# Performance work log

Hardware: AMD Instinct MI355X
Metric: run time of the kernel (lower is better)

## Reference

```python
import jax, jax.numpy as jnp
import numpy as np

B, S, H = 2, 2048, 2048
NH, KVH, HD = 32, 8, 64
G = NH // KVH
BASE = 10000.0
SCALE = 1.0 / np.sqrt(HD).astype(np.float32)


def _rope_cache(seq_len, dim, base):
    inv_freq = 1.0 / (base ** (jnp.arange(0, dim, 2, dtype=jnp.float32) / dim))
    t = jnp.arange(seq_len, dtype=jnp.float32)
    freqs = jnp.outer(t, inv_freq)            # [S, HD/2]
    emb = jnp.concatenate([freqs, freqs], -1)  # [S, HD]
    return jnp.cos(emb), jnp.sin(emb)


def _rotate_half(x):
    x1, x2 = jnp.split(x, 2, axis=-1)
    return jnp.concatenate([-x2, x1], axis=-1)


def setup_inputs() -> dict:
    key = jax.random.key(0)
    ks = jax.random.split(key, 5)
    hidden_states = jax.random.normal(ks[0], (B, S, H), jnp.float32)
    # additive causal mask, broadcast over heads
    causal = jnp.tril(jnp.ones((S, S), dtype=bool))
    attention_mask = jnp.where(causal, 0.0, -1e9).astype(jnp.float32)[None, None]
    attention_mask = jnp.broadcast_to(attention_mask, (B, 1, S, S))
    position_ids = jnp.broadcast_to(jnp.arange(S, dtype=jnp.int32), (B, S))
    w = 0.02
    Wq = jax.random.normal(ks[1], (H, NH * HD), jnp.float32) * w
    Wk = jax.random.normal(ks[2], (H, KVH * HD), jnp.float32) * w
    Wv = jax.random.normal(ks[3], (H, KVH * HD), jnp.float32) * w
    Wo = jax.random.normal(ks[4], (NH * HD, H), jnp.float32) * w
    return {"hidden_states": hidden_states, "attention_mask": attention_mask,
            "position_ids": position_ids, "Wq": Wq, "Wk": Wk, "Wv": Wv, "Wo": Wo}


def reference(hidden_states, attention_mask, position_ids, Wq, Wk, Wv, Wo):
    b, s, _ = hidden_states.shape
    q = (hidden_states @ Wq).reshape(b, s, NH, HD).transpose(0, 2, 1, 3)   # [B,NH,S,HD]
    k = (hidden_states @ Wk).reshape(b, s, KVH, HD).transpose(0, 2, 1, 3)  # [B,KVH,S,HD]
    v = (hidden_states @ Wv).reshape(b, s, KVH, HD).transpose(0, 2, 1, 3)
    cos_c, sin_c = _rope_cache(s, HD, BASE)
    cos = cos_c[position_ids][:, None]  # [B,1,S,HD]
    sin = sin_c[position_ids][:, None]
    q = q * cos + _rotate_half(q) * sin
    k = k * cos + _rotate_half(k) * sin
    # GQA: grouped einsum == repeat_kv + matmul (same math, no KV duplication)
    qg = q.reshape(b, KVH, G, s, HD)
    scores = jnp.einsum('bkgsd,bktd->bkgst', qg, k) * SCALE  # [B,KVH,G,S,S]
    scores = scores + attention_mask[:, :, None]             # mask [B,1,1,S,S]
    probs = jax.nn.softmax(scores.astype(jnp.float32), axis=-1).astype(q.dtype)
    ctx = jnp.einsum('bkgst,bktd->bkgsd', probs, v)
    ctx = ctx.reshape(b, NH, s, HD).transpose(0, 2, 1, 3).reshape(b, s, NH * HD)
    return ctx @ Wo
```

## Files before the change

kernel.cpp:

```cpp
#include <hip/hip_runtime.h>
#include <hip/hip_bf16.h>

#define DB   2
#define DS   2048
#define DH   2048
#define DNH  32
#define DKVH 8
#define DHD  64
#define DM   4096
#define DNQKV 3072

typedef __attribute__((ext_vector_type(8))) short bf16x8;
typedef __attribute__((ext_vector_type(4))) float f32x4;
typedef __attribute__((ext_vector_type(8))) unsigned short us8;
typedef __attribute__((ext_vector_type(4))) unsigned short us4;
typedef __attribute__((ext_vector_type(2))) unsigned int u32x2;

__device__ __forceinline__ float b2f(unsigned short u) {
  unsigned int x = ((unsigned int)u) << 16;
  return __builtin_bit_cast(float, x);
}
__device__ __forceinline__ unsigned short f2b(float f) {
  unsigned int u = __builtin_bit_cast(unsigned int, f);
  return (unsigned short)((u + 0x8000u) >> 16);
}
__device__ __forceinline__ unsigned int cvt_pk_bf16(float lo, float hi) {
  unsigned int r;
  asm("v_cvt_pk_bf16_f32 %0, %1, %2" : "=v"(r) : "v"(lo), "v"(hi));
  return r;
}
__device__ __forceinline__ void async_copy16(void* lds, const void* g) {
  __builtin_amdgcn_global_load_lds((const __attribute__((address_space(1))) void*)g,
                                   (__attribute__((address_space(3))) void*)lds,
                                   16, 0, 0);
}

#define BARRIER() do { asm volatile("" ::: "memory"); __builtin_amdgcn_s_barrier(); asm volatile("" ::: "memory"); } while (0)
#define LGKM0()   asm volatile("s_waitcnt lgkmcnt(0)" ::: "memory")
#define WAITVM(n) asm volatile("s_waitcnt vmcnt(" #n ")" ::: "memory")
#define MFMA16(d, a, bb) (d) = __builtin_amdgcn_mfma_f32_16x16x32_bf16((a), (bb), (d), 0, 0, 0)

__device__ __forceinline__ int detect_inline(const unsigned short* __restrict__ w) {
  int t = threadIdx.x & 63;
  int trips = 0;
#pragma unroll
  for (int i = 0; i < 4; i++) {
    unsigned short u = w[t * 4 + i];
    int e = (u >> 7) & 0xFF;
    if (e >= 161 || (e <= 93 && e != 0)) trips++;
  }
#pragma unroll
  for (int off = 32; off > 0; off >>= 1) trips += __shfl_down(trips, off);
  return __shfl(trips, 0) >= 8;
}

__global__ __launch_bounds__(256)
void prep(const void* __restrict__ hs, const void* __restrict__ wq,
          const void* __restrict__ wk, const void* __restrict__ wv,
          const void* __restrict__ wo,
          unsigned short* __restrict__ xb, unsigned short* __restrict__ wtqkv,
          unsigned short* __restrict__ wto) {
  __shared__ float tile[32][33];
  int mode = detect_inline((const unsigned short*)wq);
  int bid = blockIdx.x;
  if (bid < 4096) {
    int i = (bid * 256 + threadIdx.x) * 8;
    if (mode) {
      const float* f = (const float*)hs;
      us8 o;
#pragma unroll
      for (int j = 0; j < 8; j++) o[j] = f2b(f[i + j]);
      *(us8*)&xb[i] = o;
    } else {
      *(us8*)&xb[i] = *(const us8*)((const unsigned short*)hs + i);
    }
    return;
  }
  const void* win; unsigned short* out; int C, bx, by;
  if (bid < 8192)       { int l = bid - 4096;  win = wq; out = wtqkv;                         C = 2048; bx = l & 63; by = l >> 6; }
  else if (bid < 9216)  { int l = bid - 8192;  win = wk; out = wtqkv + (size_t)2048 * 2048;   C = 512;  bx = l & 15; by = l >> 4; }
  else if (bid < 10240) { int l = bid - 9216;  win = wv; out = wtqkv + (size_t)2560 * 2048;   C = 512;  bx = l & 15; by = l >> 4; }
  else                  { int l = bid - 10240; win = wo; out = wto;                           C = 2048; bx = l & 63; by = l >> 6; }
  int c0 = bx * 32, r0 = by * 32;
  int tx = threadIdx.x & 31, ty = threadIdx.x >> 5;
  if (mode) {
    const float* f = (const float*)win;
    for (int i = ty; i < 32; i += 8) tile[i][tx] = f[(size_t)(r0 + i) * C + c0 + tx];
  } else {
    const unsigned short* bsrc = (const unsigned short*)win;
    for (int i = ty; i < 32; i += 8) tile[i][tx] = b2f(bsrc[(size_t)(r0 + i) * C + c0 + tx]);
  }
  __syncthreads();
  for (int i = ty; i < 32; i += 8) out[(size_t)(c0 + i) * 2048 + r0 + tx] = f2b(tile[tx][i]);
}

#define QSC 0.18033688011112042f

__global__ __launch_bounds__(512, 2)
void gemm_qkv(const unsigned short* __restrict__ A, const unsigned short* __restrict__ Bt,
              const int* __restrict__ pos_ids,
              unsigned short* __restrict__ qws, unsigned short* __restrict__ kws,
              unsigned short* __restrict__ vt) {
  __shared__ __align__(16) unsigned short sm[65536];
  int tid = threadIdx.x, lane = tid & 63, wave = tid >> 6;
  int wm = wave >> 2, wn = wave & 3;
  int quad = lane >> 4, l15 = lane & 15;

  int bid = blockIdx.x;
  int wg = (bid & 7) * 24 + (bid >> 3);
  int ty = wg / 12, tx = wg - ty * 12;
  size_t tm0 = (size_t)ty * 256, tn0 = (size_t)tx * 256;

  const unsigned short* Ab = A + tm0 * 2048;
  const unsigned short* Bb = Bt + tn0 * 2048;

  auto UA = [&](int bu, int kh) { return sm + (bu * 2 + kh) * 8192; };
  auto UB = [&](int bu, int kh) { return sm + 32768 + (bu * 2 + kh) * 8192; };

  int c0 = tid, c1 = tid + 512;
  int r0s = c0 >> 2, r1s = c1 >> 2;
  int cc0 = (c0 & 3) ^ ((r0s >> 1) & 3);
  int cc1 = (c1 & 3) ^ ((r1s >> 1) & 3);
  size_t ga0 = (size_t)r0s * 2048 + cc0 * 8;
  size_t ga1 = (size_t)r1s * 2048 + cc1 * 8;

  auto stA = [&](int t, int kh, int bu) {
    const unsigned short* s = Ab + (size_t)t * 64 + kh * 32;
    async_copy16(UA(bu, kh) + c0 * 8, s + ga0);
    async_copy16(UA(bu, kh) + c1 * 8, s + ga1);
  };
  auto stB = [&](int t, int kh, int bu) {
    const unsigned short* s = Bb + (size_t)t * 64 + kh * 32;
    async_copy16(UB(bu, kh) + c0 * 8, s + ga0);
    async_copy16(UB(bu, kh) + c1 * 8, s + ga1);
  };

  int rdoff = l15 * 32 + ((quad << 3) ^ (((l15 >> 1) & 3) << 3));

  f32x4 zero4 = {0.f, 0.f, 0.f, 0.f};
  f32x4 acc[8][4];
#pragma unroll
  for (int mi = 0; mi < 8; mi++)
#pragma unroll
    for (int ni = 0; ni < 4; ni++) acc[mi][ni] = zero4;

  stA(0, 0, 0); stB(0, 0, 0); stA(0, 1, 0); stB(0, 1, 0); stA(1, 0, 1); stB(1, 0, 1);
  WAITVM(8); BARRIER();

#pragma unroll 2
  for (int t = 0; t < 32; ++t) {
    int bu = t & 1, bn = bu ^ 1;
    int t1 = (t + 1 < 32) ? t + 1 : 31;
    int t2 = (t + 2 < 32) ? t + 2 : 31;
    bf16x8 af[8];
    const unsigned short* pA0 = UA(bu, 0) + wm * 4096 + rdoff;
    const unsigned short* pB0 = UB(bu, 0) + wn * 2048 + rdoff;
    const unsigned short* pA1 = UA(bu, 1) + wm * 4096 + rdoff;
    const unsigned short* pB1 = UB(bu, 1) + wn * 2048 + rdoff;

#pragma unroll
    for (int mi = 0; mi < 8; mi++) af[mi] = *(const bf16x8*)(pA0 + mi * 512);
    bf16x8 b0 = *(const bf16x8*)pB0;
    bf16x8 b1 = *(const bf16x8*)(pB0 + 512);
    stA(t1, 1, bn);
    BARRIER(); LGKM0();
    __builtin_amdgcn_s_setprio(1);
#pragma unroll
    for (int mi = 0; mi < 8; mi++) { MFMA16(acc[mi][0], af[mi], b0); MFMA16(acc[mi][1], af[mi], b1); }
    __builtin_amdgcn_s_setprio(0);
    BARRIER();

    bf16x8 b2 = *(const bf16x8*)(pB0 + 1024);
    bf16x8 b3 = *(const bf16x8*)(pB0 + 1536);
    stB(t1, 1, bn);
    BARRIER(); LGKM0();
    __builtin_amdgcn_s_setprio(1);
#pragma unroll
    for (int mi = 0; mi < 8; mi++) { MFMA16(acc[mi][2], af[mi], b2); MFMA16(acc[mi][3], af[mi], b3); }
    __builtin_amdgcn_s_setprio(0);
    WAITVM(8);
    BARRIER();

#pragma unroll
    for (int mi = 0; mi < 8; mi++) af[mi] = *(const bf16x8*)(pA1 + mi * 512);
    b0 = *(const bf16x8*)pB1;
    b1 = *(const bf16x8*)(pB1 + 512);
    stA(t2, 0, bu);
    BARRIER(); LGKM0();
    __builtin_amdgcn_s_setprio(1);
#pragma unroll
    for (int mi = 0; mi < 8; mi++) { MFMA16(acc[mi][0], af[mi], b0); MFMA16(acc[mi][1], af[mi], b1); }
    __builtin_amdgcn_s_setprio(0);
    BARRIER();

    b2 = *(const bf16x8*)(pB1 + 1024);
    b3 = *(const bf16x8*)(pB1 + 1536);
    stB(t2, 0, bu);
    BARRIER(); LGKM0();
    __builtin_amdgcn_s_setprio(1);
#pragma unroll
    for (int mi = 0; mi < 8; mi++) { MFMA16(acc[mi][2], af[mi], b2); MFMA16(acc[mi][3], af[mi], b3); }
    __builtin_amdgcn_s_setprio(0);
    WAITVM(8);
    BARRIER();
  }
  WAITVM(0);

  int hs = (int)(tn0 >> 6) + wn;
  if (hs < 40) {
    float sc = (hs < 32) ? QSC : 1.0f;
    unsigned short* dst0 = (hs < 32) ? qws : kws;
    int hh = (hs < 32) ? hs : (hs - 32);
    float invf0 = __expf(-(float)l15 * (9.210340371976184f / 32.0f));
    float invf1 = invf0 * 0.01f;
#pragma unroll
    for (int mi = 0; mi < 8; mi++)
#pragma unroll
      for (int r = 0; r < 4; r++) {
        size_t gr = tm0 + wm * 128 + mi * 16 + quad * 4 + r;
        int bb = (int)(gr >> 11), s = (int)(gr & 2047);
        float tpos = (float)pos_ids[gr];
        unsigned short* row = dst0 + ((size_t)(bb * ((hs < 32) ? DNH : DKVH) + hh) * DS + s) * DHD;
#pragma unroll
        for (int ni = 0; ni < 2; ni++) {
          float x1 = acc[mi][ni][r], x2 = acc[mi][ni + 2][r];
          float ang = tpos * (ni ? invf1 : invf0);
          float sn, cs;
          __sincosf(ang, &sn, &cs);
          int d = ni * 16 + l15;
          row[d]      = f2b((x1 * cs - x2 * sn) * sc);
          row[d + 32] = f2b((x2 * cs + x1 * sn) * sc);
        }
      }
  } else {
    int vh = hs - 40;
    int bb = (int)(tm0 >> 11);
    int s0 = (int)(tm0 & 2047) + wm * 128 + quad * 4;
#pragma unroll
    for (int mi = 0; mi < 8; mi++)
#pragma unroll
      for (int ni = 0; ni < 4; ni++) {
        int d = ni * 16 + l15;
        us4 o4;
#pragma unroll
        for (int r = 0; r < 4; r++) o4[r] = f2b(acc[mi][ni][r]);
        *(us4*)&vt[((size_t)(bb * DKVH + vh) * DHD + d) * DS + s0 + mi * 16] = o4;
      }
  }
}

__global__ __launch_bounds__(512, 2)
void gemm_out(const unsigned short* __restrict__ A, const unsigned short* __restrict__ Bt,
              unsigned short* __restrict__ Cb, float* __restrict__ Cf,
              const unsigned short* __restrict__ wqdet) {
  __shared__ __align__(16) unsigned short sm[49152];
  int tid = threadIdx.x, lane = tid & 63, wave = tid >> 6;
  int wm = wave >> 2, wn = wave & 3;
  int quad = lane >> 4, l15 = lane & 15;

  int bid = blockIdx.x;
  int wg = (bid & 7) * 32 + (bid >> 3);
  int ty = wg >> 3, tx = wg & 7;
  size_t tm0 = (size_t)ty * 128, tn0 = (size_t)tx * 256;

  const unsigned short* Ab = A + tm0 * 2048;
  const unsigned short* Bb = Bt + tn0 * 2048;

  auto UA = [&](int bu, int kh) { return sm + (bu * 2 + kh) * 4096; };
  auto UB = [&](int bu, int kh) { return sm + 16384 + (bu * 2 + kh) * 8192; };

  int c0 = tid, c1 = tid + 512;
  int r0s = c0 >> 2, r1s = c1 >> 2;
  int cc0 = (c0 & 3) ^ ((r0s >> 1) & 3);
  int cc1 = (c1 & 3) ^ ((r1s >> 1) & 3);
  size_t ga0 = (size_t)r0s * 2048 + cc0 * 8;
  size_t ga1 = (size_t)r1s * 2048 + cc1 * 8;

  auto stA = [&](int t, int kh, int bu) {
    const unsigned short* s = Ab + (size_t)t * 64 + kh * 32;
    async_copy16(UA(bu, kh) + c0 * 8, s + ga0);
  };
  auto stB = [&](int t, int kh, int bu) {
    const unsigned short* s = Bb + (size_t)t * 64 + kh * 32;
    async_copy16(UB(bu, kh) + c0 * 8, s + ga0);
    async_copy16(UB(bu, kh) + c1 * 8, s + ga1);
  };

  int rdoff = l15 * 32 + ((quad << 3) ^ (((l15 >> 1) & 3) << 3));

  f32x4 zero4 = {0.f, 0.f, 0.f, 0.f};
  f32x4 acc[4][4];
#pragma unroll
  for (int mi = 0; mi < 4; mi++)
#pragma unroll
    for (int ni = 0; ni < 4; ni++) acc[mi][ni] = zero4;

  stA(0, 0, 0); stB(0, 0, 0); stA(0, 1, 0); stB(0, 1, 0); stA(1, 0, 1); stB(1, 0, 1);
  WAITVM(6); BARRIER();

#pragma unroll 2
  for (int t = 0; t < 32; ++t) {
    int bu = t & 1, bn = bu ^ 1;
    int t1 = (t + 1 < 32) ? t + 1 : 31;
    int t2 = (t + 2 < 32) ? t + 2 : 31;
    bf16x8 af[4];
    const unsigned short* pA0 = UA(bu, 0) + wm * 2048 + rdoff;
    const unsigned short* pB0 = UB(bu, 0) + wn * 2048 + rdoff;
    const unsigned short* pA1 = UA(bu, 1) + wm * 2048 + rdoff;
    const unsigned short* pB1 = UB(bu, 1) + wn * 2048 + rdoff;

#pragma unroll
    for (int mi = 0; mi < 4; mi++) af[mi] = *(const bf16x8*)(pA0 + mi * 512);
    bf16x8 b0 = *(const bf16x8*)pB0;
    bf16x8 b1 = *(const bf16x8*)(pB0 + 512);
    stA(t1, 1, bn);
    BARRIER(); LGKM0();
    __builtin_amdgcn_s_setprio(1);
#pragma unroll
    for (int mi = 0; mi < 4; mi++) { MFMA16(acc[mi][0], af[mi], b0); MFMA16(acc[mi][1], af[mi], b1); }
    __builtin_amdgcn_s_setprio(0);
    BARRIER();

    bf16x8 b2 = *(const bf16x8*)(pB0 + 1024);
    bf16x8 b3 = *(const bf16x8*)(pB0 + 1536);
    stB(t1, 1, bn);
    BARRIER(); LGKM0();
    __builtin_amdgcn_s_setprio(1);
#pragma unroll
    for (int mi = 0; mi < 4; mi++) { MFMA16(acc[mi][2], af[mi], b2); MFMA16(acc[mi][3], af[mi], b3); }
    __builtin_amdgcn_s_setprio(0);
    WAITVM(6);
    BARRIER();

#pragma unroll
    for (int mi = 0; mi < 4; mi++) af[mi] = *(const bf16x8*)(pA1 + mi * 512);
    b0 = *(const bf16x8*)pB1;
    b1 = *(const bf16x8*)(pB1 + 512);
    stA(t2, 0, bu);
    BARRIER(); LGKM0();
    __builtin_amdgcn_s_setprio(1);
#pragma unroll
    for (int mi = 0; mi < 4; mi++) { MFMA16(acc[mi][0], af[mi], b0); MFMA16(acc[mi][1], af[mi], b1); }
    __builtin_amdgcn_s_setprio(0);
    BARRIER();

    b2 = *(const bf16x8*)(pB1 + 1024);
    b3 = *(const bf16x8*)(pB1 + 1536);
    stB(t2, 0, bu);
    BARRIER(); LGKM0();
    __builtin_amdgcn_s_setprio(1);
#pragma unroll
    for (int mi = 0; mi < 4; mi++) { MFMA16(acc[mi][2], af[mi], b2); MFMA16(acc[mi][3], af[mi], b3); }
    __builtin_amdgcn_s_setprio(0);
    WAITVM(6);
    BARRIER();
  }
  WAITVM(0);

  int mode = detect_inline(wqdet);
#pragma unroll
  for (int mi = 0; mi < 4; mi++)
#pragma unroll
    for (int ni = 0; ni < 4; ni++)
#pragma unroll
      for (int r = 0; r < 4; r++) {
        size_t gr = tm0 + wm * 64 + mi * 16 + quad * 4 + r;
        size_t gc = tn0 + wn * 64 + ni * 16 + l15;
        float v = acc[mi][ni][r];
        if (mode) Cf[gr * 2048 + gc] = v;
        else      Cb[gr * 2048 + gc] = f2b(v);
      }
}

__global__ __launch_bounds__(256, 4)
void flash_attn(const unsigned short* __restrict__ q, const unsigned short* __restrict__ k,
                const unsigned short* __restrict__ vt, unsigned short* __restrict__ ctx) {
  __shared__ __align__(16) unsigned short lK[2][2][64 * 32];
  __shared__ __align__(16) unsigned short lV[2][2][64 * 32];
  __shared__ __align__(16) unsigned short lP[4][16 * 64];
  int tid = threadIdx.x, lane = tid & 63, wave = tid >> 6;
  int quad = lane >> 4, l15 = lane & 15;
  int bh = blockIdx.y, b = bh >> 5, h = bh & 31, kvh = h >> 2;
  const unsigned short* qb = q + (size_t)(b * DNH + h) * DS * DHD;
  const unsigned short* kb = k + (size_t)(b * DKVH + kvh) * DS * DHD;
  const unsigned short* vb = vt + (size_t)(b * DKVH + kvh) * DHD * DS;
  unsigned short* lPw = lP[wave];
  int r4 = tid >> 2;
  int cc8 = ((tid & 3) ^ ((r4 >> 1) & 3)) * 8;
  int swz = ((l15 >> 1) & 3) << 3;
  int pswz = (l15 & 7) << 3;
  int ql = wave * 16 + l15;

  int qt = blockIdx.x;
  int ntA = qt + 1, ntB = 32 - qt;
  int q0A = qt * 64, q0B = (31 - qt) * 64;

  const unsigned short* qpA = qb + (size_t)(q0A + ql) * DHD + quad * 8;
  const unsigned short* qpB = qb + (size_t)(q0B + ql) * DHD + quad * 8;
  bf16x8 qfA0 = *(const bf16x8*)qpA;
  bf16x8 qfA1 = *(const bf16x8*)(qpA + 32);
  bf16x8 qfB0 = *(const bf16x8*)qpB;
  bf16x8 qfB1 = *(const bf16x8*)(qpB + 32);

  f32x4 zero4 = {0.f, 0.f, 0.f, 0.f};
  f32x4 oA[4], oB[4];
#pragma unroll
  for (int dj = 0; dj < 4; dj++) { oA[dj] = zero4; oB[dj] = zero4; }
  float mA = -1e30f, lA = 0.f, mB = -1e30f, lB = 0.f;

  auto stage = [&](int t, int buf) {
    const unsigned short* sk = kb + (size_t)(t * 64 + r4) * DHD + cc8;
    async_copy16(&lK[buf][0][tid * 8], sk);
    async_copy16(&lK[buf][1][tid * 8], sk + 32);
    const unsigned short* sv = vb + (size_t)r4 * DS + t * 64 + cc8;
    async_copy16(&lV[buf][0][tid * 8], sv);
    async_copy16(&lV[buf][1][tid * 8], sv + 32);
  };

  auto smax_pv = [&](f32x4 (&sacc)[4], float& mrow, float& lrow, f32x4 (&oacc)[4],
                     int cur, int maskdiag) {
    if (maskdiag) {
#pragma unroll
      for (int nj = 0; nj < 4; nj++)
#pragma unroll
        for (int r = 0; r < 4; r++)
          if (nj * 16 + quad * 4 + r > ql) sacc[nj][r] = -1e30f;
    }
    float a0 = fmaxf(fmaxf(sacc[0][0], sacc[0][1]), sacc[0][2]);
    float a1 = fmaxf(fmaxf(sacc[0][3], sacc[1][0]), sacc[1][1]);
    float a2 = fmaxf(fmaxf(sacc[1][2], sacc[1][3]), sacc[2][0]);
    float a3 = fmaxf(fmaxf(sacc[2][1], sacc[2][2]), sacc[2][3]);
    float a4 = fmaxf(fmaxf(sacc[3][0], sacc[3][1]), sacc[3][2]);
    float tm = fmaxf(fmaxf(fmaxf(a0, a1), fmaxf(a2, a3)), fmaxf(a4, sacc[3][3]));
    tm = fmaxf(tm, __shfl_xor(tm, 16));
    tm = fmaxf(tm, __shfl_xor(tm, 32));
    if (!__all(tm <= mrow + 8.f)) {
      float mn = fmaxf(mrow, tm);
      float alpha = __builtin_amdgcn_exp2f(mrow - mn);
      mrow = mn;
      lrow *= alpha;
#pragma unroll
      for (int dj = 0; dj < 4; dj++)
#pragma unroll
        for (int r = 0; r < 4; r++) oacc[dj][r] *= alpha;
    }
    float rs = 0.f;
#pragma unroll
    for (int nj = 0; nj < 4; nj++)
#pragma unroll
      for (int r = 0; r < 4; r++) {
        float e = __builtin_amdgcn_exp2f(sacc[nj][r] - mrow);
        sacc[nj][r] = e;
        rs += e;
      }
    rs += __shfl_xor(rs, 16);
    rs += __shfl_xor(rs, 32);
    lrow += rs;
#pragma unroll
    for (int nj = 0; nj < 4; nj++) {
      u32x2 w2;
      w2[0] = cvt_pk_bf16(sacc[nj][0], sacc[nj][1]);
      w2[1] = cvt_pk_bf16(sacc[nj][2], sacc[nj][3]);
      *(u32x2*)&lPw[l15 * 64 + ((nj * 16 + quad * 4) ^ pswz)] = w2;
    }
    bf16x8 pf0 = *(const bf16x8*)&lPw[l15 * 64 + ((quad * 8) ^ pswz)];
    bf16x8 pf1 = *(const bf16x8*)&lPw[l15 * 64 + ((32 + quad * 8) ^ pswz)];
    __builtin_amdgcn_s_setprio(1);
#pragma unroll
    for (int dj = 0; dj < 4; dj++) {
      int ro = (dj * 16 + l15) * 32 + ((quad * 8) ^ swz);
      bf16x8 vf0 = *(const bf16x8*)&lV[cur][0][ro];
      bf16x8 vf1 = *(const bf16x8*)&lV[cur][1][ro];
      MFMA16(oacc[dj], vf0, pf0);
      MFMA16(oacc[dj], vf1, pf1);
    }
    __builtin_amdgcn_s_setprio(0);
  };

  stage(0, 0);
  WAITVM(0); BARRIER();

  int cur = 0;
  for (int t = 0; t < ntA; t++) {
    stage(t + 1, cur ^ 1);
    f32x4 sA[4], sB[4];
    __builtin_amdgcn_s_setprio(1);
#pragma unroll
    for (int nj = 0; nj < 4; nj++) {
      int ro = (nj * 16 + l15) * 32 + ((quad * 8) ^ swz);
      bf16x8 kf0 = *(const bf16x8*)&lK[cur][0][ro];
      bf16x8 kf1 = *(const bf16x8*)&lK[cur][1][ro];
      sA[nj] = zero4;
      MFMA16(sA[nj], kf0, qfA0);
      MFMA16(sA[nj], kf1, qfA1);
      sB[nj] = zero4;
      MFMA16(sB[nj], kf0, qfB0);
      MFMA16(sB[nj], kf1, qfB1);
    }
    __builtin_amdgcn_s_setprio(0);
    smax_pv(sA, mA, lA, oA, cur, t == ntA - 1);
    smax_pv(sB, mB, lB, oB, cur, 0);
    WAITVM(0); BARRIER();
    cur ^= 1;
  }
  for (int t = ntA; t < ntB; t++) {
    if (t + 1 < ntB) stage(t + 1, cur ^ 1);
    f32x4 sB[4];
    __builtin_amdgcn_s_setprio(1);
#pragma unroll
    for (int nj = 0; nj < 4; nj++) {
      int ro = (nj * 16 + l15) * 32 + ((quad * 8) ^ swz);
      bf16x8 kf0 = *(const bf16x8*)&lK[cur][0][ro];
      bf16x8 kf1 = *(const bf16x8*)&lK[cur][1][ro];
      sB[nj] = zero4;
      MFMA16(sB[nj], kf0, qfB0);
      MFMA16(sB[nj], kf1, qfB1);
    }
    __builtin_amdgcn_s_setprio(0);
    smax_pv(sB, mB, lB, oB, cur, t == ntB - 1);
    WAITVM(0); BARRIER();
    cur ^= 1;
  }

  auto wout = [&](f32x4 (&oacc)[4], float lrow, int q0) {
    float inv = __builtin_amdgcn_rcpf(lrow);
    size_t orow = ((size_t)b * DS + q0 + ql) * (DNH * DHD) + (size_t)h * DHD;
#pragma unroll
    for (int dj = 0; dj < 4; dj++) {
      u32x2 o2;
      o2[0] = cvt_pk_bf16(oacc[dj][0] * inv, oacc[dj][1] * inv);
      o2[1] = cvt_pk_bf16(oacc[dj][2] * inv, oacc[dj][3] * inv);
      *(u32x2*)&ctx[orow + dj * 16 + quad * 4] = o2;
    }
  };
  wout(oA, lA, q0A);
  wout(oB, lB, q0B);
}

extern "C" void kernel_launch(void* const* d_in, const int* in_sizes, int n_in,
                              void* d_out, int out_size, void* d_ws, size_t ws_size,
                              hipStream_t stream) {
  (void)in_sizes; (void)n_in; (void)out_size; (void)ws_size;
  const void* hs = d_in[0];
  const int* pos = (const int*)d_in[2];
  const void* wq = d_in[3];
  const void* wk = d_in[4];
  const void* wv = d_in[5];
  const void* wo = d_in[6];

  char* ws = (char*)d_ws;
  size_t off = 0;
  auto take = [&](size_t bytes) -> char* {
    char* p = ws + off;
    off += (bytes + 255) & ~(size_t)255;
    return p;
  };
  unsigned short* xb    = (unsigned short*)take((size_t)DM * DH * 2);
  unsigned short* wtqkv = (unsigned short*)take((size_t)DNQKV * DH * 2);
  unsigned short* wto   = (unsigned short*)take((size_t)DH * DH * 2);
  unsigned short* qws   = (unsigned short*)take((size_t)DB * DNH * DS * DHD * 2);
  unsigned short* kws   = (unsigned short*)take((size_t)DB * DKVH * DS * DHD * 2);
  unsigned short* vtws  = (unsigned short*)take((size_t)DB * DKVH * DS * DHD * 2);
  unsigned short* ctx   = (unsigned short*)take((size_t)DM * DNH * DHD * 2);

  prep<<<14336, 256, 0, stream>>>(hs, wq, wk, wv, wo, xb, wtqkv, wto);

  gemm_qkv<<<dim3(192), 512, 0, stream>>>(xb, wtqkv, pos, qws, kws, vtws);

  flash_attn<<<dim3(16, DB * DNH), 256, 0, stream>>>(qws, kws, vtws, ctx);

  gemm_out<<<dim3(256), 512, 0, stream>>>(ctx, wto, (unsigned short*)d_out, (float*)d_out,
                                          (const unsigned short*)wq);
}
```

Measured before the change: 306.6 us.

## Use 128-row query tiles with 8 waves per flash-attention block

Flash attention blocks grow from 4 to 8 waves, each covering 128 query rows per paired tile instead of 64. Each staged K/V tile is shared by twice as many waves, which halves per-thread copy work and K/V traffic per query row. The causal mask now uses a general row-versus-column compare so the diagonal tiles of 128-row groups are handled. The grid is reordered so the head index runs along x, which changes block scheduling, and there are half as many blocks, so occupancy and load balance may suffer.

```diff
diff --git a/kernel.cpp b/kernel.cpp
--- a/kernel.cpp
+++ b/kernel.cpp
@@ -372,35 +372,34 @@
       }
 }
 
-__global__ __launch_bounds__(256, 4)
+__global__ __launch_bounds__(512, 4)
 void flash_attn(const unsigned short* __restrict__ q, const unsigned short* __restrict__ k,
                 const unsigned short* __restrict__ vt, unsigned short* __restrict__ ctx) {
   __shared__ __align__(16) unsigned short lK[2][2][64 * 32];
   __shared__ __align__(16) unsigned short lV[2][2][64 * 32];
-  __shared__ __align__(16) unsigned short lP[4][16 * 64];
+  __shared__ __align__(16) unsigned short lP[8][16 * 64];
   int tid = threadIdx.x, lane = tid & 63, wave = tid >> 6;
   int quad = lane >> 4, l15 = lane & 15;
-  int bh = blockIdx.y, b = bh >> 5, h = bh & 31, kvh = h >> 2;
+  int bh = blockIdx.x, b = bh >> 5, h = bh & 31, kvh = h >> 2;
   const unsigned short* qb = q + (size_t)(b * DNH + h) * DS * DHD;
   const unsigned short* kb = k + (size_t)(b * DKVH + kvh) * DS * DHD;
   const unsigned short* vb = vt + (size_t)(b * DKVH + kvh) * DHD * DS;
   unsigned short* lPw = lP[wave];
-  int r4 = tid >> 2;
-  int cc8 = ((tid & 3) ^ ((r4 >> 1) & 3)) * 8;
+  int shalf = tid >> 8, r8 = tid & 255;
+  int rowS = r8 >> 2;
+  int cc8 = ((r8 & 3) ^ ((rowS >> 1) & 3)) * 8;
   int swz = ((l15 >> 1) & 3) << 3;
   int pswz = (l15 & 7) << 3;
   int ql = wave * 16 + l15;
 
-  int qt = blockIdx.x;
-  int ntA = qt + 1, ntB = 32 - qt;
-  int q0A = qt * 64, q0B = (31 - qt) * 64;
-
-  const unsigned short* qpA = qb + (size_t)(q0A + ql) * DHD + quad * 8;
-  const unsigned short* qpB = qb + (size_t)(q0B + ql) * DHD + quad * 8;
-  bf16x8 qfA0 = *(const bf16x8*)qpA;
-  bf16x8 qfA1 = *(const bf16x8*)(qpA + 32);
-  bf16x8 qfB0 = *(const bf16x8*)qpB;
-  bf16x8 qfB1 = *(const bf16x8*)(qpB + 32);
+  int qt = blockIdx.y;
+  int ntA = 2 * qt + 2, ntB = 32 - 2 * qt;
+  int qAg = qt * 128 + ql, qBg = (15 - qt) * 128 + ql;
+
+  const unsigned short* qpA = qb + (size_t)qAg * DHD + quad * 8;
+  const unsigned short* qpB = qb + (size_t)qBg * DHD + quad * 8;
+  bf16x8 qfA0 = *(const bf16x8*)qpA, qfA1 = *(const bf16x8*)(qpA + 32);
+  bf16x8 qfB0 = *(const bf16x8*)qpB, qfB1 = *(const bf16x8*)(qpB + 32);
 
   f32x4 zero4 = {0.f, 0.f, 0.f, 0.f};
   f32x4 oA[4], oB[4];
@@ -409,22 +408,20 @@
   float mA = -1e30f, lA = 0.f, mB = -1e30f, lB = 0.f;
 
   auto stage = [&](int t, int buf) {
-    const unsigned short* sk = kb + (size_t)(t * 64 + r4) * DHD + cc8;
-    async_copy16(&lK[buf][0][tid * 8], sk);
-    async_copy16(&lK[buf][1][tid * 8], sk + 32);
-    const unsigned short* sv = vb + (size_t)r4 * DS + t * 64 + cc8;
-    async_copy16(&lV[buf][0][tid * 8], sv);
-    async_copy16(&lV[buf][1][tid * 8], sv + 32);
+    const unsigned short* sk = kb + (size_t)(t * 64 + rowS) * DHD + shalf * 32 + cc8;
+    async_copy16(&lK[buf][shalf][r8 * 8], sk);
+    const unsigned short* sv = vb + (size_t)rowS * DS + t * 64 + shalf * 32 + cc8;
+    async_copy16(&lV[buf][shalf][r8 * 8], sv);
   };
 
   auto smax_pv = [&](f32x4 (&sacc)[4], float& mrow, float& lrow, f32x4 (&oacc)[4],
-                     int cur, int maskdiag) {
-    if (maskdiag) {
+                     int cur, int kv0, int qg, bool domask) {
+    if (domask) {
 #pragma unroll
       for (int nj = 0; nj < 4; nj++)
 #pragma unroll
         for (int r = 0; r < 4; r++)
-          if (nj * 16 + quad * 4 + r > ql) sacc[nj][r] = -1e30f;
+          if (kv0 + nj * 16 + quad * 4 + r > qg) sacc[nj][r] = -1e30f;
     }
     float a0 = fmaxf(fmaxf(sacc[0][0], sacc[0][1]), sacc[0][2]);
     float a1 = fmaxf(fmaxf(sacc[0][3], sacc[1][0]), sacc[1][1]);
@@ -498,8 +495,8 @@
       MFMA16(sB[nj], kf1, qfB1);
     }
     __builtin_amdgcn_s_setprio(0);
-    smax_pv(sA, mA, lA, oA, cur, t == ntA - 1);
-    smax_pv(sB, mB, lB, oB, cur, 0);
+    smax_pv(sA, mA, lA, oA, cur, t * 64, qAg, (t * 64 + 63) > qAg);
+    smax_pv(sB, mB, lB, oB, cur, t * 64, qBg, false);
     WAITVM(0); BARRIER();
     cur ^= 1;
   }
@@ -517,14 +514,14 @@
       MFMA16(sB[nj], kf1, qfB1);
     }
     __builtin_amdgcn_s_setprio(0);
-    smax_pv(sB, mB, lB, oB, cur, t == ntB - 1);
+    smax_pv(sB, mB, lB, oB, cur, t * 64, qBg, (t * 64 + 63) > qBg);
     WAITVM(0); BARRIER();
     cur ^= 1;
   }
 
-  auto wout = [&](f32x4 (&oacc)[4], float lrow, int q0) {
+  auto wout = [&](f32x4 (&oacc)[4], float lrow, int qg) {
     float inv = __builtin_amdgcn_rcpf(lrow);
-    size_t orow = ((size_t)b * DS + q0 + ql) * (DNH * DHD) + (size_t)h * DHD;
+    size_t orow = ((size_t)b * DS + qg) * (DNH * DHD) + (size_t)h * DHD;
 #pragma unroll
     for (int dj = 0; dj < 4; dj++) {
       u32x2 o2;
@@ -533,8 +530,8 @@
       *(u32x2*)&ctx[orow + dj * 16 + quad * 4] = o2;
     }
   };
-  wout(oA, lA, q0A);
-  wout(oB, lB, q0B);
+  wout(oA, lA, qAg);
+  wout(oB, lB, qBg);
 }
 
 extern "C" void kernel_launch(void* const* d_in, const int* in_sizes, int n_in,
@@ -567,7 +564,7 @@
 
   gemm_qkv<<<dim3(192), 512, 0, stream>>>(xb, wtqkv, pos, qws, kws, vtws);
 
-  flash_attn<<<dim3(16, DB * DNH), 256, 0, stream>>>(qws, kws, vtws, ctx);
+  flash_attn<<<dim3(DB * DNH, 8), 512, 0, stream>>>(qws, kws, vtws, ctx);
 
   gemm_out<<<dim3(256), 512, 0, stream>>>(ctx, wto, (unsigned short*)d_out, (float*)d_out,
                                           (const unsigned short*)wq);
```

Measured after the change: 300.4 us. 1.02x faster.
